# Kernel tuning notes

Hardware: AMD Instinct MI355X
Metric: run time of the kernel (lower is better)

The kernel has to match this reference:

```python
import jax, jax.numpy as jnp
import numpy as np

B, P, D, N, H = 1, 256, 512, 8, 64
STD = 0.02
IGNORE = -1000000.0


def setup_inputs() -> dict:
    key = jax.random.key(0)
    ks = jax.random.split(key, 9)
    inp = {"normalized_resid_pre": jax.random.normal(ks[0], (B, P, D), jnp.float32)}
    for i, s in enumerate("ABCDE"):
        inp["W_" + s] = STD * jax.random.normal(ks[i + 1], (N, D, H), jnp.float32)
        inp["b_" + s] = jnp.zeros((N, H), jnp.float32)
    inp["W_V"] = STD * jax.random.normal(ks[6], (N, H, H, H), jnp.float32)
    inp["W_K"] = STD * jax.random.normal(ks[7], (N, H, H, H), jnp.float32)
    inp["W_O"] = STD * jax.random.normal(ks[8], (N, H, D), jnp.float32)
    inp["b_O"] = jnp.zeros((D,), jnp.float32)
    return inp


def reference(normalized_resid_pre, W_A, b_A, W_B, b_B, W_C, b_C, W_D, b_D, W_E, b_E, W_V, W_K, W_O, b_O):
    x = normalized_resid_pre
    b_sz = x.shape[0]
    proj = lambda W, b: jnp.einsum('ndh,bpd->bpnh', W, x) + b
    ta = proj(W_A, b_A)
    tb = proj(W_B, b_B)
    tc = proj(W_C, b_C)
    td = proj(W_D, b_D)
    te = proj(W_E, b_E)
    # V_Layer: v[b, p1, p2, n, h3]
    v = jnp.einsum('bpnh,bqng,nhgf->bpqnf', td, te, W_V)
    # TrittentionCScore: chained einsums -> scores[b, n, p, q, r]
    step1 = jnp.einsum('brnk,nijk->brij', tc, W_K)
    step2 = jnp.einsum('brij,bqnj->briq', step1, tb)
    scores = jnp.einsum('briq,bpni->bnpqr', step2, ta)
    # CausalMask (attn_eq=False, order_attn=True): mask over (t=p, s=q, q=r) dims
    ti = jnp.arange(P)[:, None, None]
    si = jnp.arange(P)[None, :, None]
    qi = jnp.arange(P)[None, None, :]
    mask = (ti >= qi) | (si >= qi) | (ti >= si)  # [P, P, P]
    scores = jnp.where(mask, IGNORE, scores)
    # TrittentionCPattern: b n p q r -> b n r (p q), /d_head, extra column, softmax
    flat = jnp.transpose(scores, (0, 1, 4, 2, 3)).reshape(b_sz, N, P, P * P) / H
    extra = jnp.full((b_sz, N, P, 1), -1000.0, flat.dtype)
    attn = jax.nn.softmax(jnp.concatenate([flat, extra], axis=-1), axis=-1)
    # Z_Layer: v -> b n h (p s), extra zero column, combine
    vf = jnp.transpose(v, (0, 3, 4, 1, 2)).reshape(b_sz, N, H, P * P)
    vf = jnp.concatenate([vf, jnp.zeros((b_sz, N, H, 1), vf.dtype)], axis=-1)
    z = jnp.einsum('bnql,bnhl->bqnh', attn, vf)
    # Result + Out
    zint = jnp.einsum('bqnh,nhd->bqnd', z, W_O)
    return zint.sum(axis=2) + b_O
```

## Files before the change

### kernel.cpp

```cpp
#include <hip/hip_runtime.h>
#include <hip/hip_bf16.h>


typedef __hip_bfloat16 bf16;
typedef __attribute__((ext_vector_type(8))) short short8;
typedef __attribute__((ext_vector_type(4))) short s16x4;
typedef __attribute__((ext_vector_type(4))) float floatx4;

__device__ __forceinline__ float ldf(const float* p){ return *p; }
__device__ __forceinline__ float ldf(const bf16* p){ return __bfloat162float(*p); }
__device__ __forceinline__ void  stf(float* p, float v){ *p = v; }
__device__ __forceinline__ void  stf(bf16*  p, float v){ *p = __float2bfloat16(v); }

__device__ __forceinline__ floatx4 mfma16(short8 a, short8 b, floatx4 c){
  return __builtin_amdgcn_mfma_f32_16x16x32_bf16(a, b, c, 0, 0, 0);
}
__device__ __forceinline__ short8 ld_g8(const bf16* p){
  return *reinterpret_cast<const short8*>(p);
}
__device__ __forceinline__ short bfs(float x){
  bf16 v = __float2bfloat16(x);
  return *reinterpret_cast<short*>(&v);
}

__device__ __forceinline__ bool is_bf16_x(const void* xv)
{
  const unsigned* x32 = (const unsigned*)xv;
  unsigned w = x32[threadIdx.x & 63];
  unsigned lo = w & 0xFFFFu;
  unsigned e  = (lo >> 7) & 0xFFu;
  bool v = (lo == 0u) || (e >= 90u && e <= 145u);
  unsigned long long m = __ballot(v);
  return __popcll(m) >= 40;
}

template<typename TI>
__device__ __forceinline__ void proj_body(
    const TI* __restrict__ x, const TI* const* Ws, const TI* const* bs,
    bf16* __restrict__ tproj, float* As, float* Bs)
{
  const int bz = blockIdx.z, j = bz >> 3, n = bz & 7;
  const TI* B    = Ws[j] + (size_t)n * 32768;
  const TI* bias = bs[j] + n * 64;
  bf16* out = tproj + (size_t)j * 131072;
  const int m0 = blockIdx.y * 64;
  const int t = threadIdx.x, tx = t & 15, ty = t >> 4;
  float acc[4][4] = {};
  for (int k0 = 0; k0 < 512; k0 += 16) {
    { int m = t >> 2, kk = (t & 3) * 4;
      const TI* ap = x + (size_t)(m0 + m) * 512 + (k0 + kk);
      float a0 = ldf(ap+0), a1 = ldf(ap+1), a2 = ldf(ap+2), a3 = ldf(ap+3);
      As[(kk+0)*68+m] = a0; As[(kk+1)*68+m] = a1;
      As[(kk+2)*68+m] = a2; As[(kk+3)*68+m] = a3; }
    { int kk = t >> 4, nn = (t & 15) * 4;
      const TI* bp = B + (size_t)(k0 + kk) * 64 + nn;
      Bs[kk*68+nn+0] = ldf(bp+0); Bs[kk*68+nn+1] = ldf(bp+1);
      Bs[kk*68+nn+2] = ldf(bp+2); Bs[kk*68+nn+3] = ldf(bp+3); }
    __syncthreads();
    #pragma unroll
    for (int kk = 0; kk < 16; kk++) {
      float4 a4 = *reinterpret_cast<const float4*>(&As[kk*68 + ty*4]);
      float4 b4 = *reinterpret_cast<const float4*>(&Bs[kk*68 + tx*4]);
      float av[4] = {a4.x,a4.y,a4.z,a4.w}, bv[4] = {b4.x,b4.y,b4.z,b4.w};
      #pragma unroll
      for (int im = 0; im < 4; im++)
        #pragma unroll
        for (int in = 0; in < 4; in++) acc[im][in] += av[im] * bv[in];
    }
    __syncthreads();
  }
  #pragma unroll
  for (int im = 0; im < 4; im++)
    #pragma unroll
    for (int in = 0; in < 4; in++) {
      float v = acc[im][in] + ldf(bias + tx*4 + in);
      int p = m0 + ty*4 + im, h = tx*4 + in;
      if (j < 3) out[(size_t)p * 512 + n*64 + h] = __float2bfloat16(v);
      else       out[(size_t)n * 16384 + (size_t)h * 256 + p] = __float2bfloat16(v);
    }
}

__global__ __launch_bounds__(256) void proj_all(
    const void* __restrict__ x,
    const void* W0, const void* b0, const void* W1, const void* b1,
    const void* W2, const void* b2, const void* W3, const void* b3,
    const void* W4, const void* b4, bf16* __restrict__ tproj)
{
  __shared__ float As[16*68];
  __shared__ float Bs[16*68];
  if (is_bf16_x(x)) {
    const bf16* Ws[5] = {(const bf16*)W0,(const bf16*)W1,(const bf16*)W2,
                         (const bf16*)W3,(const bf16*)W4};
    const bf16* bs[5] = {(const bf16*)b0,(const bf16*)b1,(const bf16*)b2,
                         (const bf16*)b3,(const bf16*)b4};
    proj_body<bf16>((const bf16*)x, Ws, bs, tproj, As, Bs);
  } else {
    const float* Ws[5] = {(const float*)W0,(const float*)W1,(const float*)W2,
                          (const float*)W3,(const float*)W4};
    const float* bs[5] = {(const float*)b0,(const float*)b1,(const float*)b2,
                          (const float*)b3,(const float*)b4};
    proj_body<float>((const float*)x, Ws, bs, tproj, As, Bs);
  }
}

template<typename TW>
__device__ __forceinline__ void s1t_body(
    const bf16* __restrict__ tc, const TW* __restrict__ WK,
    bf16* __restrict__ s1t)
{
  const int i = blockIdx.x;
  const int t = threadIdx.x, wid = t >> 6, lane = t & 63, quad = lane >> 4, l16 = lane & 15;
  const int rw = blockIdx.y * 64 + wid * 16;
  floatx4 acc[4];
  #pragma unroll
  for (int jt = 0; jt < 4; jt++) acc[jt] = (floatx4){0.f, 0.f, 0.f, 0.f};
  for (int kc = 0; kc < 16; kc++) {
    short8 af = ld_g8(tc + (size_t)(rw + l16) * 512 + kc*32 + quad*8);
    const int n = kc >> 1, kk = (kc & 1) * 32 + quad * 8;
    #pragma unroll
    for (int jt = 0; jt < 4; jt++) {
      const TW* bp = WK + ((size_t)(n*64 + i) * 64 + jt*16 + l16) * 64 + kk;
      short8 bf;
      if constexpr (sizeof(TW) == 2) {
        bf = ld_g8((const bf16*)bp);
      } else {
        float4 x0 = *reinterpret_cast<const float4*>(bp);
        float4 x1 = *reinterpret_cast<const float4*>(bp + 4);
        bf[0]=bfs(x0.x); bf[1]=bfs(x0.y); bf[2]=bfs(x0.z); bf[3]=bfs(x0.w);
        bf[4]=bfs(x1.x); bf[5]=bfs(x1.y); bf[6]=bfs(x1.z); bf[7]=bfs(x1.w);
      }
      acc[jt] = mfma16(af, bf, acc[jt]);
    }
  }
  #pragma unroll
  for (int jt = 0; jt < 4; jt++)
    #pragma unroll
    for (int reg = 0; reg < 4; reg++)
      s1t[(size_t)(rw + quad*4 + reg) * 4096 + i*64 + jt*16 + l16] =
          __float2bfloat16(acc[jt][reg]);
}

__global__ __launch_bounds__(256) void s1t_all(
    const void* __restrict__ x, const bf16* __restrict__ tb,
    const bf16* __restrict__ tc, const void* __restrict__ WK,
    bf16* __restrict__ tbsbf, bf16* __restrict__ s1t)
{
  if (blockIdx.y == 4) {
    int t = blockIdx.x * 256 + threadIdx.x;
    int q = t >> 6, j = t & 63;
    float s = 0.f;
    #pragma unroll
    for (int n = 0; n < 8; n++) s += ldf(tb + q*512 + n*64 + j);
    tbsbf[t] = __float2bfloat16(s * 0.015625f);
    return;
  }
  if (is_bf16_x(x)) s1t_body<bf16>(tc, (const bf16*)WK, s1t);
  else              s1t_body<float>(tc, (const float*)WK, s1t);
}

#define E_PHASE(PT, BUF)                                                      \
  {                                                                           \
    const int ptb_ = ((PT)*4 + wid) * 16;                                     \
    for (int qt2 = 0; qt2 < 2; qt2++) {                                       \
      const int qh = qc + qt2*16;                                             \
      char* erow0 = (BUF) + (quad*4)*72 + (qt2*16 + l16)*2;                   \
      if (qh + 15 <= ptb_) {                                                  \
        for (int reg = 0; reg < 4; reg++)                                     \
          *reinterpret_cast<bf16*>(erow0 + reg*72) = __float2bfloat16(0.f);   \
      } else {                                                                \
        floatx4 acc = {0.f, 0.f, 0.f, 0.f};                                   \
        acc = mfma16(taf[PT][0], cfr[qt2][0], acc);                           \
        acc = mfma16(taf[PT][1], cfr[qt2][1], acc);                           \
        if (qh >= ptb_ + 16 && qh + 15 < r) {                                 \
          for (int reg = 0; reg < 4; reg++) {                                 \
            float e = __expf(acc[reg]);                                       \
            Zp += e;                                                          \
            *reinterpret_cast<bf16*>(erow0 + reg*72) = __float2bfloat16(e);   \
          }                                                                   \
        } else {                                                              \
          for (int reg = 0; reg < 4; reg++) {                                 \
            int p = ptb_ + quad*4 + reg;                                      \
            int q = qh + l16;                                                 \
            float e = (p < q && q < r) ? __expf(acc[reg]) : 0.f;              \
            Zp += e;                                                          \
            *reinterpret_cast<bf16*>(erow0 + reg*72) = __float2bfloat16(e);   \
          }                                                                   \
        }                                                                     \
      }                                                                       \
    }                                                                         \
  }

__global__ __launch_bounds__(256) void tri_attn(
    const bf16* __restrict__ ta,
    const bf16* __restrict__ tbsbf,
    const bf16* __restrict__ s1t,
    const bf16* __restrict__ tdT,
    const bf16* __restrict__ teT,
    bf16* __restrict__ Sbuf)
{
  __shared__ __align__(16) char smb[44544];
  const int bx = blockIdx.x;
  const int n = bx & 7;
  const int r = 255 - (bx >> 3);
  const int t = threadIdx.x;
  const int wid = t >> 6, lane = t & 63, quad = lane >> 4, l16 = lane & 15;
  bf16* srow = Sbuf + (size_t)n * 1048576 + (size_t)r * 4096;
  if (r < 2) {
    short8 zz = (short8){0,0,0,0,0,0,0,0};
    reinterpret_cast<short8*>(srow)[t]       = zz;
    reinterpret_cast<short8*>(srow)[t + 256] = zz;
    return;
  }
  const int nch  = ((r - 1) >> 5) + 1;
  const int rcap = nch * 32;

  {
    const bf16* s1r = s1t + (size_t)r * 4096;
    short8 bfr[4][2];
    #pragma unroll
    for (int it = 0; it < 4; it++)
      #pragma unroll
      for (int kc = 0; kc < 2; kc++)
        bfr[it][kc] = ld_g8(s1r + (it*16 + l16)*64 + kc*32 + quad*8);
    #pragma unroll
    for (int qt = 0; qt < 4; qt++) {
      const int q0 = wid * 64 + qt * 16;
      if (q0 >= rcap) continue;
      if (q0 >= r) {
        #pragma unroll
        for (int it = 0; it < 4; it++)
          #pragma unroll
          for (int reg = 0; reg < 4; reg++) {
            int q = q0 + quad*4 + reg;
            *reinterpret_cast<bf16*>(smb + q*136 + (it*16 + l16)*2) =
                __float2bfloat16(0.f);
          }
        continue;
      }
      short8 af0 = ld_g8(tbsbf + (q0 + l16)*64 + quad*8);
      short8 af1 = ld_g8(tbsbf + (q0 + l16)*64 + 32 + quad*8);
      #pragma unroll
      for (int it = 0; it < 4; it++) {
        floatx4 acc = {0.f, 0.f, 0.f, 0.f};
        acc = mfma16(af0, bfr[it][0], acc);
        acc = mfma16(af1, bfr[it][1], acc);
        #pragma unroll
        for (int reg = 0; reg < 4; reg++) {
          int q = q0 + quad*4 + reg;
          float v = (q >= 1 && q < r) ? acc[reg] : 0.f;
          *reinterpret_cast<bf16*>(smb + q*136 + (it*16 + l16)*2) = __float2bfloat16(v);
        }
      }
    }
  }
  short8 taf[4][2];
  #pragma unroll
  for (int pt = 0; pt < 4; pt++)
    #pragma unroll
    for (int kc = 0; kc < 2; kc++)
      taf[pt][kc] = ld_g8(ta + (size_t)((pt*4 + wid)*16 + l16)*512 + n*64
                             + kc*32 + quad*8);
  __syncthreads();

  floatx4 Tacc[4][4];
  #pragma unroll
  for (int pt = 0; pt < 4; pt++)
    #pragma unroll
    for (int gt = 0; gt < 4; gt++) Tacc[pt][gt] = (floatx4){0.f, 0.f, 0.f, 0.f};
  float Zp = 0.f;
  char* bufA = smb + 34816 + wid * 2304;
  char* bufB = bufA + 1152;
  for (int ch = 0; ch < nch; ch++) {
    const int qc = ch * 32;
    if (qc + 31 <= wid * 16) continue;
    short8 cfr[2][2];
    #pragma unroll
    for (int qt2 = 0; qt2 < 2; qt2++)
      #pragma unroll
      for (int kc = 0; kc < 2; kc++)
        cfr[qt2][kc] = *reinterpret_cast<const short8*>(
            smb + (qc + qt2*16 + l16)*136 + (kc*32 + quad*8)*2);
    short8 tef[4];
    #pragma unroll
    for (int gt = 0; gt < 4; gt++)
      tef[gt] = ld_g8(teT + (size_t)n*16384 + (gt*16 + l16)*256 + qc + quad*8);

    {
      const bool alive0 = ((0*4 + wid)*16 < qc + 31);
      const bool alive1 = ((1*4 + wid)*16 < qc + 31);
      short8 ef0, ef1;
      if (alive0) { E_PHASE(0, bufA)
                    ef0 = *reinterpret_cast<const short8*>(bufA + l16*72 + quad*16); }
      if (alive1) { E_PHASE(1, bufB)
                    ef1 = *reinterpret_cast<const short8*>(bufB + l16*72 + quad*16); }
      if (alive0) { __builtin_amdgcn_s_setprio(1);
        #pragma unroll
        for (int gt = 0; gt < 4; gt++) Tacc[0][gt] = mfma16(ef0, tef[gt], Tacc[0][gt]);
        __builtin_amdgcn_s_setprio(0); }
      if (alive1) { __builtin_amdgcn_s_setprio(1);
        #pragma unroll
        for (int gt = 0; gt < 4; gt++) Tacc[1][gt] = mfma16(ef1, tef[gt], Tacc[1][gt]);
        __builtin_amdgcn_s_setprio(0); }
    }
    {
      const bool alive2 = ((2*4 + wid)*16 < qc + 31);
      const bool alive3 = ((3*4 + wid)*16 < qc + 31);
      short8 ef2, ef3;
      if (alive2) { E_PHASE(2, bufA)
                    ef2 = *reinterpret_cast<const short8*>(bufA + l16*72 + quad*16); }
      if (alive3) { E_PHASE(3, bufB)
                    ef3 = *reinterpret_cast<const short8*>(bufB + l16*72 + quad*16); }
      if (alive2) { __builtin_amdgcn_s_setprio(1);
        #pragma unroll
        for (int gt = 0; gt < 4; gt++) Tacc[2][gt] = mfma16(ef2, tef[gt], Tacc[2][gt]);
        __builtin_amdgcn_s_setprio(0); }
      if (alive3) { __builtin_amdgcn_s_setprio(1);
        #pragma unroll
        for (int gt = 0; gt < 4; gt++) Tacc[3][gt] = mfma16(ef3, tef[gt], Tacc[3][gt]);
        __builtin_amdgcn_s_setprio(0); }
    }
  }
  #pragma unroll
  for (int off = 32; off; off >>= 1) Zp += __shfl_down(Zp, off);
  float* scr = reinterpret_cast<float*>(smb + 44032);
  if (lane == 0) scr[wid] = Zp;
  __syncthreads();
  const float rinv = 1.f / (scr[0] + scr[1] + scr[2] + scr[3]);

  #pragma unroll
  for (int pt = 0; pt < 4; pt++) {
    if ((pt*4 + wid)*16 >= rcap) continue;
    #pragma unroll
    for (int gt = 0; gt < 4; gt++)
      #pragma unroll
      for (int reg = 0; reg < 4; reg++) {
        int g = gt*16 + l16;
        int p = (pt*4 + wid)*16 + quad*4 + reg;
        *reinterpret_cast<bf16*>(smb + g*528 + p*2) = __float2bfloat16(Tacc[pt][gt][reg]);
      }
  }
  __syncthreads();

  {
    short8 Taf[8];
    #pragma unroll
    for (int kc = 0; kc < 8; kc++)
      if (kc < nch)
        Taf[kc] = *reinterpret_cast<const short8*>(
            smb + (wid*16 + l16)*528 + (kc*32 + quad*8)*2);
    #pragma unroll
    for (int ht = 0; ht < 4; ht++) {
      floatx4 acc = {0.f, 0.f, 0.f, 0.f};
      __builtin_amdgcn_s_setprio(1);
      #pragma unroll
      for (int kc = 0; kc < 8; kc++) {
        if (kc < nch) {
          short8 bfragd = ld_g8(tdT + (size_t)n*16384 + (ht*16 + l16)*256 + kc*32 + quad*8);
          acc = mfma16(Taf[kc], bfragd, acc);
        }
      }
      __builtin_amdgcn_s_setprio(0);
      #pragma unroll
      for (int reg = 0; reg < 4; reg++) {
        int g = wid*16 + quad*4 + reg, h = ht*16 + l16;
        srow[h*64 + g] = __float2bfloat16(acc[reg] * rinv);
      }
    }
  }
}

template<typename TW>
__device__ __forceinline__ void z_body(
    const bf16* __restrict__ Sbuf, const TW* __restrict__ WV,
    float* __restrict__ zpart, int kslice, char* lds)
{
  const int rt = blockIdx.x, n = blockIdx.y, ks = blockIdx.z;
  const int t = threadIdx.x, wid = t >> 6, lane = t & 63, quad = lane >> 4, l16 = lane & 15;
  const int rw = rt * 64 + wid * 16;
  const int k0 = ks * kslice;
  const TW*  wvn = WV   + (size_t)n * 262144;
  const bf16* sn = Sbuf + (size_t)n * 1048576;
  floatx4 acc[4];
  #pragma unroll
  for (int ft = 0; ft < 4; ft++) acc[ft] = (floatx4){0.f, 0.f, 0.f, 0.f};
  const int row = t >> 3, f8 = (t & 7) * 8;
  for (int kb = k0; kb < k0 + kslice; kb += 32) {
    { const TW* src = wvn + (size_t)(kb + row) * 64 + f8;
      short sv[8];
      if constexpr (sizeof(TW) == 2) {
        short8 v = ld_g8((const bf16*)src);
        #pragma unroll
        for (int j = 0; j < 8; j++) sv[j] = v[j];
      } else {
        float4 a = *reinterpret_cast<const float4*>(src);
        float4 b = *reinterpret_cast<const float4*>(src + 4);
        sv[0]=bfs(a.x); sv[1]=bfs(a.y); sv[2]=bfs(a.z); sv[3]=bfs(a.w);
        sv[4]=bfs(b.x); sv[5]=bfs(b.y); sv[6]=bfs(b.z); sv[7]=bfs(b.w);
      }
      short* dst = reinterpret_cast<short*>(lds + row*136 + f8*2);
      s16x4 lo = {sv[0],sv[1],sv[2],sv[3]}, hi = {sv[4],sv[5],sv[6],sv[7]};
      *reinterpret_cast<s16x4*>(dst)     = lo;
      *reinterpret_cast<s16x4*>(dst + 4) = hi;
    }
    __syncthreads();
    short8 af = ld_g8(sn + (size_t)(rw + l16) * 4096 + kb + quad*8);
    #pragma unroll
    for (int ft = 0; ft < 4; ft++) {
      short8 bfv;
      #pragma unroll
      for (int j = 0; j < 8; j++)
        bfv[j] = *reinterpret_cast<const short*>(
            lds + (quad*8 + j)*136 + (ft*16 + l16)*2);
      acc[ft] = mfma16(af, bfv, acc[ft]);
    }
    __syncthreads();
  }
  float* zp = zpart + (size_t)ks * 131072;
  #pragma unroll
  for (int ft = 0; ft < 4; ft++)
    #pragma unroll
    for (int reg = 0; reg < 4; reg++)
      zp[(size_t)(rw + quad*4 + reg) * 512 + n*64 + ft*16 + l16] = acc[ft][reg];
}

__global__ __launch_bounds__(256) void z_all(
    const void* __restrict__ x, const bf16* __restrict__ Sbuf,
    const void* __restrict__ WV, float* __restrict__ zpart, int kslice)
{
  __shared__ __align__(16) char lds[32 * 136];
  if (is_bf16_x(x)) z_body<bf16>(Sbuf, (const bf16*)WV, zpart, kslice, lds);
  else              z_body<float>(Sbuf, (const float*)WV, zpart, kslice, lds);
}

__global__ __launch_bounds__(256) void zred_kern(
    const float* __restrict__ zpart, bf16* __restrict__ zbb, int ks)
{
  int idx = blockIdx.x * 256 + threadIdx.x;
  float s = 0.f;
  for (int k = 0; k < ks; k++) s += zpart[(size_t)k * 131072 + idx];
  zbb[idx] = __float2bfloat16(s);
}

template<typename TB, typename TC>
__device__ __forceinline__ void gemm_body(
    const bf16* __restrict__ A, const TB* __restrict__ B, TC* __restrict__ C,
    const TB* __restrict__ bias, float* As, float* Bs)
{
  const int m0 = blockIdx.y * 64, n0 = blockIdx.x * 64;
  const int t = threadIdx.x, tx = t & 15, ty = t >> 4;
  float acc[4][4] = {};
  for (int k0 = 0; k0 < 512; k0 += 16) {
    { int m = t >> 2, kk = (t & 3) * 4;
      const bf16* ap = A + (size_t)(m0 + m) * 512 + (k0 + kk);
      float a0 = ldf(ap+0), a1 = ldf(ap+1), a2 = ldf(ap+2), a3 = ldf(ap+3);
      As[(kk+0)*68+m] = a0; As[(kk+1)*68+m] = a1;
      As[(kk+2)*68+m] = a2; As[(kk+3)*68+m] = a3; }
    { int kk = t >> 4, nn = (t & 15) * 4;
      const TB* bp = B + (size_t)(k0 + kk) * 512 + (n0 + nn);
      Bs[kk*68+nn+0] = ldf(bp+0); Bs[kk*68+nn+1] = ldf(bp+1);
      Bs[kk*68+nn+2] = ldf(bp+2); Bs[kk*68+nn+3] = ldf(bp+3); }
    __syncthreads();
    #pragma unroll
    for (int kk = 0; kk < 16; kk++) {
      float4 a4 = *reinterpret_cast<const float4*>(&As[kk*68 + ty*4]);
      float4 b4 = *reinterpret_cast<const float4*>(&Bs[kk*68 + tx*4]);
      float av[4] = {a4.x,a4.y,a4.z,a4.w}, bv[4] = {b4.x,b4.y,b4.z,b4.w};
      #pragma unroll
      for (int im = 0; im < 4; im++)
        #pragma unroll
        for (int in = 0; in < 4; in++) acc[im][in] += av[im] * bv[in];
    }
    __syncthreads();
  }
  #pragma unroll
  for (int im = 0; im < 4; im++) {
    TC* cp = C + (size_t)(m0 + ty*4 + im) * 512 + n0 + tx*4;
    #pragma unroll
    for (int in = 0; in < 4; in++) {
      float v = acc[im][in] + ldf(bias + n0 + tx*4 + in);
      stf(cp + in, v);
    }
  }
}

__global__ __launch_bounds__(256) void gemm_all(
    const void* __restrict__ x, const bf16* __restrict__ zbb,
    const void* __restrict__ WO, const void* __restrict__ bO,
    void* __restrict__ out)
{
  __shared__ float As[16*68];
  __shared__ float Bs[16*68];
  if (is_bf16_x(x))
    gemm_body<bf16, bf16>(zbb, (const bf16*)WO, (bf16*)out, (const bf16*)bO, As, Bs);
  else
    gemm_body<float, float>(zbb, (const float*)WO, (float*)out, (const float*)bO, As, Bs);
}

extern "C" void kernel_launch(void* const* d_in, const int* in_sizes, int n_in,
                              void* d_out, int out_size, void* d_ws, size_t ws_size,
                              hipStream_t stream)
{
  (void)in_sizes; (void)n_in; (void)out_size;
  char* wsb = (char*)d_ws;
  bf16* tproj = (bf16*)(wsb + 256);
  bf16* tbsbf = (bf16*)(wsb + 1310976);
  bf16* s1t   = (bf16*)(wsb + 1343744);
  bf16* zbb   = (bf16*)(wsb + 3440896);
  bf16* Sbuf  = (bf16*)(wsb + 4194304);
  const long TE = 131072;
  const bool bigws = (ws_size == 0) || (ws_size >= 25165824);
  const int  ks     = bigws ? 8 : 2;
  const int  kslice = 4096 / ks;
  float* zpart = (float*)(bigws ? (wsb + 20971520) : (wsb + 1343744));

  proj_all<<<dim3(1,4,40), 256, 0, stream>>>(
      d_in[0], d_in[1], d_in[2], d_in[3], d_in[4], d_in[5], d_in[6],
      d_in[7], d_in[8], d_in[9], d_in[10], tproj);
  s1t_all<<<dim3(64,5), 256, 0, stream>>>(
      d_in[0], tproj + 1*TE, tproj + 2*TE, d_in[12], tbsbf, s1t);
  tri_attn<<<2048, 256, 0, stream>>>(
      tproj, tbsbf, s1t, tproj + 3*TE, tproj + 4*TE, Sbuf);
  z_all<<<dim3(4,8,ks), 256, 0, stream>>>(
      d_in[0], Sbuf, d_in[11], zpart, kslice);
  zred_kern<<<512, 256, 0, stream>>>(zpart, zbb, ks);
  gemm_all<<<dim3(8,4), 256, 0, stream>>>(
      d_in[0], zbb, d_in[13], d_in[14], d_out);
}
```

Baseline: 254.2 us.

## Increase block counts for z and output GEMM kernels, vectorize projection loads

The z kernel now gives each wave a different 16-column output slice of the same 16 rows instead of 16 rows by 64 columns, which multiplies the grid by four. The final output GEMM shrinks its tiles from 64x64 to 32x32, which multiplies its grid by four. The projection kernel loads four elements per vector load instead of four scalar loads. The aim is to fill more compute units in small, latency-bound kernels. The cost is more redundant loads of the shared operand per block and less reuse per thread.

```diff
diff --git a/kernel.cpp b/kernel.cpp
--- a/kernel.cpp
+++ b/kernel.cpp
@@ -21,6 +21,17 @@
 __device__ __forceinline__ short bfs(float x){
   bf16 v = __float2bfloat16(x);
   return *reinterpret_cast<short*>(&v);
+}
+
+__device__ __forceinline__ void ld4(const bf16* p, float* o){
+  s16x4 v = *reinterpret_cast<const s16x4*>(p);
+  #pragma unroll
+  for (int i = 0; i < 4; i++)
+    o[i] = __uint_as_float(((unsigned)(unsigned short)v[i]) << 16);
+}
+__device__ __forceinline__ void ld4(const float* p, float* o){
+  float4 v = *reinterpret_cast<const float4*>(p);
+  o[0] = v.x; o[1] = v.y; o[2] = v.z; o[3] = v.w;
 }
 
 __device__ __forceinline__ bool is_bf16_x(const void* xv)
@@ -48,14 +59,13 @@
   float acc[4][4] = {};
   for (int k0 = 0; k0 < 512; k0 += 16) {
     { int m = t >> 2, kk = (t & 3) * 4;
-      const TI* ap = x + (size_t)(m0 + m) * 512 + (k0 + kk);
-      float a0 = ldf(ap+0), a1 = ldf(ap+1), a2 = ldf(ap+2), a3 = ldf(ap+3);
-      As[(kk+0)*68+m] = a0; As[(kk+1)*68+m] = a1;
-      As[(kk+2)*68+m] = a2; As[(kk+3)*68+m] = a3; }
+      float a[4]; ld4(x + (size_t)(m0 + m) * 512 + (k0 + kk), a);
+      As[(kk+0)*68+m] = a[0]; As[(kk+1)*68+m] = a[1];
+      As[(kk+2)*68+m] = a[2]; As[(kk+3)*68+m] = a[3]; }
     { int kk = t >> 4, nn = (t & 15) * 4;
-      const TI* bp = B + (size_t)(k0 + kk) * 64 + nn;
-      Bs[kk*68+nn+0] = ldf(bp+0); Bs[kk*68+nn+1] = ldf(bp+1);
-      Bs[kk*68+nn+2] = ldf(bp+2); Bs[kk*68+nn+3] = ldf(bp+3); }
+      float b[4]; ld4(B + (size_t)(k0 + kk) * 64 + nn, b);
+      Bs[kk*68+nn+0] = b[0]; Bs[kk*68+nn+1] = b[1];
+      Bs[kk*68+nn+2] = b[2]; Bs[kk*68+nn+3] = b[3]; }
     __syncthreads();
     #pragma unroll
     for (int kk = 0; kk < 16; kk++) {
@@ -376,13 +386,11 @@
 {
   const int rt = blockIdx.x, n = blockIdx.y, ks = blockIdx.z;
   const int t = threadIdx.x, wid = t >> 6, lane = t & 63, quad = lane >> 4, l16 = lane & 15;
-  const int rw = rt * 64 + wid * 16;
+  const int rw = rt * 16;
   const int k0 = ks * kslice;
   const TW*  wvn = WV   + (size_t)n * 262144;
   const bf16* sn = Sbuf + (size_t)n * 1048576;
-  floatx4 acc[4];
-  #pragma unroll
-  for (int ft = 0; ft < 4; ft++) acc[ft] = (floatx4){0.f, 0.f, 0.f, 0.f};
+  floatx4 acc = {0.f, 0.f, 0.f, 0.f};
   const int row = t >> 3, f8 = (t & 7) * 8;
   for (int kb = k0; kb < k0 + kslice; kb += 32) {
     { const TW* src = wvn + (size_t)(kb + row) * 64 + f8;
@@ -404,23 +412,18 @@
     }
     __syncthreads();
     short8 af = ld_g8(sn + (size_t)(rw + l16) * 4096 + kb + quad*8);
-    #pragma unroll
-    for (int ft = 0; ft < 4; ft++) {
-      short8 bfv;
-      #pragma unroll
-      for (int j = 0; j < 8; j++)
-        bfv[j] = *reinterpret_cast<const short*>(
-            lds + (quad*8 + j)*136 + (ft*16 + l16)*2);
-      acc[ft] = mfma16(af, bfv, acc[ft]);
-    }
+    short8 bfv;
+    #pragma unroll
+    for (int j = 0; j < 8; j++)
+      bfv[j] = *reinterpret_cast<const short*>(
+          lds + (quad*8 + j)*136 + (wid*16 + l16)*2);
+    acc = mfma16(af, bfv, acc);
     __syncthreads();
   }
   float* zp = zpart + (size_t)ks * 131072;
   #pragma unroll
-  for (int ft = 0; ft < 4; ft++)
-    #pragma unroll
-    for (int reg = 0; reg < 4; reg++)
-      zp[(size_t)(rw + quad*4 + reg) * 512 + n*64 + ft*16 + l16] = acc[ft][reg];
+  for (int reg = 0; reg < 4; reg++)
+    zp[(size_t)(rw + quad*4 + reg) * 512 + n*64 + wid*16 + l16] = acc[reg];
 }
 
 __global__ __launch_bounds__(256) void z_all(
@@ -446,38 +449,32 @@
     const bf16* __restrict__ A, const TB* __restrict__ B, TC* __restrict__ C,
     const TB* __restrict__ bias, float* As, float* Bs)
 {
-  const int m0 = blockIdx.y * 64, n0 = blockIdx.x * 64;
+  const int m0 = blockIdx.y * 32, n0 = blockIdx.x * 32;
   const int t = threadIdx.x, tx = t & 15, ty = t >> 4;
-  float acc[4][4] = {};
+  float acc[2][2] = {};
   for (int k0 = 0; k0 < 512; k0 += 16) {
-    { int m = t >> 2, kk = (t & 3) * 4;
+    { int m = t >> 3, kk = (t & 7) * 2;
       const bf16* ap = A + (size_t)(m0 + m) * 512 + (k0 + kk);
-      float a0 = ldf(ap+0), a1 = ldf(ap+1), a2 = ldf(ap+2), a3 = ldf(ap+3);
-      As[(kk+0)*68+m] = a0; As[(kk+1)*68+m] = a1;
-      As[(kk+2)*68+m] = a2; As[(kk+3)*68+m] = a3; }
-    { int kk = t >> 4, nn = (t & 15) * 4;
+      As[(kk+0)*34+m] = ldf(ap+0); As[(kk+1)*34+m] = ldf(ap+1); }
+    { int kk = t >> 4, nn = (t & 15) * 2;
       const TB* bp = B + (size_t)(k0 + kk) * 512 + (n0 + nn);
-      Bs[kk*68+nn+0] = ldf(bp+0); Bs[kk*68+nn+1] = ldf(bp+1);
-      Bs[kk*68+nn+2] = ldf(bp+2); Bs[kk*68+nn+3] = ldf(bp+3); }
+      Bs[kk*34+nn+0] = ldf(bp+0); Bs[kk*34+nn+1] = ldf(bp+1); }
     __syncthreads();
     #pragma unroll
     for (int kk = 0; kk < 16; kk++) {
-      float4 a4 = *reinterpret_cast<const float4*>(&As[kk*68 + ty*4]);
-      float4 b4 = *reinterpret_cast<const float4*>(&Bs[kk*68 + tx*4]);
-      float av[4] = {a4.x,a4.y,a4.z,a4.w}, bv[4] = {b4.x,b4.y,b4.z,b4.w};
-      #pragma unroll
-      for (int im = 0; im < 4; im++)
-        #pragma unroll
-        for (int in = 0; in < 4; in++) acc[im][in] += av[im] * bv[in];
+      float a0 = As[kk*34 + ty*2], a1 = As[kk*34 + ty*2 + 1];
+      float b0 = Bs[kk*34 + tx*2], b1 = Bs[kk*34 + tx*2 + 1];
+      acc[0][0] += a0*b0; acc[0][1] += a0*b1;
+      acc[1][0] += a1*b0; acc[1][1] += a1*b1;
     }
     __syncthreads();
   }
   #pragma unroll
-  for (int im = 0; im < 4; im++) {
-    TC* cp = C + (size_t)(m0 + ty*4 + im) * 512 + n0 + tx*4;
-    #pragma unroll
-    for (int in = 0; in < 4; in++) {
-      float v = acc[im][in] + ldf(bias + n0 + tx*4 + in);
+  for (int im = 0; im < 2; im++) {
+    TC* cp = C + (size_t)(m0 + ty*2 + im) * 512 + n0 + tx*2;
+    #pragma unroll
+    for (int in = 0; in < 2; in++) {
+      float v = acc[im][in] + ldf(bias + n0 + tx*2 + in);
       stf(cp + in, v);
     }
   }
@@ -488,8 +485,8 @@
     const void* __restrict__ WO, const void* __restrict__ bO,
     void* __restrict__ out)
 {
-  __shared__ float As[16*68];
-  __shared__ float Bs[16*68];
+  __shared__ float As[16*34];
+  __shared__ float Bs[16*34];
   if (is_bf16_x(x))
     gemm_body<bf16, bf16>(zbb, (const bf16*)WO, (bf16*)out, (const bf16*)bO, As, Bs);
   else
@@ -520,9 +517,9 @@
       d_in[0], tproj + 1*TE, tproj + 2*TE, d_in[12], tbsbf, s1t);
   tri_attn<<<2048, 256, 0, stream>>>(
       tproj, tbsbf, s1t, tproj + 3*TE, tproj + 4*TE, Sbuf);
-  z_all<<<dim3(4,8,ks), 256, 0, stream>>>(
+  z_all<<<dim3(16,8,ks), 256, 0, stream>>>(
       d_in[0], Sbuf, d_in[11], zpart, kslice);
   zred_kern<<<512, 256, 0, stream>>>(zpart, zbb, ks);
-  gemm_all<<<dim3(8,4), 256, 0, stream>>>(
+  gemm_all<<<dim3(16,8), 256, 0, stream>>>(
       d_in[0], zbb, d_in[13], d_in[14], d_out);
 }
```

New measurement: 244.9 us. 1.04x faster.
